# Kernel tuning notes

Hardware: AMD Instinct MI355X
Metric: run time of the kernel (lower is better)

The kernel has to match this reference:

```python
import jax, jax.numpy as jnp
import numpy as np

N = 262144
C = 81
NUM_HARD = 32768


def setup_inputs() -> dict:
    key = jax.random.key(0)
    k1, k2, k3, k4 = jax.random.split(key, 4)
    return {
        "cls_score": jax.random.normal(k1, (N, C), dtype=jnp.float32),
        "rois_label": jax.random.randint(k2, (N,), 0, C, dtype=jnp.int32),
        "bbox_pred": jax.random.normal(k3, (N, 4), dtype=jnp.float32),
        "rois_target": jax.random.normal(k4, (N, 4), dtype=jnp.float32),
        "rois_inside_ws": jnp.ones((N, 4), dtype=jnp.float32),
        "rois_outside_ws": jnp.ones((N, 4), dtype=jnp.float32),
        "num_hard": NUM_HARD,
    }


def reference(cls_score, rois_label, bbox_pred, rois_target,
              rois_inside_ws, rois_outside_ws, num_hard):
    num_classes = cls_score.shape[1]
    pos = rois_label > 0                                   # [N] bool
    num_pos = jnp.sum(pos.astype(jnp.float32))

    # --- hard-example mining on detached scores (no grad through selection) ---
    conf_p = jax.lax.stop_gradient(cls_score)              # [N, C]
    x_max = jnp.max(conf_p)                                # global scalar max (as in torch code)
    lse = jnp.log(jnp.sum(jnp.exp(conf_p - x_max), axis=1)) + x_max   # [N]
    gathered = jnp.take_along_axis(conf_p, rois_label[:, None].astype(jnp.int32), axis=1)[:, 0]
    loss_c = lse - gathered                                # [N]
    loss_c = jnp.where(pos, jnp.float32(100.0), loss_c)    # force positives in
    _, topk_idx = jax.lax.top_k(loss_c, num_hard)          # [num_hard]

    # --- weighted cross entropy on selected hard examples ---
    weight = jnp.ones((num_classes,), dtype=jnp.float32).at[0].set(num_pos / num_hard)
    sel_logits = cls_score[topk_idx]                       # [num_hard, C]
    sel_labels = rois_label[topk_idx]                      # [num_hard]
    logp = jax.nn.log_softmax(sel_logits, axis=1)
    nll = -jnp.take_along_axis(logp, sel_labels[:, None].astype(jnp.int32), axis=1)[:, 0]
    w = weight[sel_labels]
    loss_cls = jnp.sum(w * nll) / jnp.sum(w)               # torch weighted-mean CE

    # --- smooth L1 on positive rois only (masked; mean over num_pos*4 elems) ---
    diff = bbox_pred - rois_target                         # [N, 4]
    ad = jnp.abs(diff)
    sl1 = jnp.where(ad < 1.0, 0.5 * diff * diff, ad - 0.5)
    posf = pos.astype(sl1.dtype)[:, None]
    loss_box = jnp.sum(sl1 * posf) / (num_pos * 4.0)

    return loss_cls, loss_box
```

## Files before the change

kernel.cpp:

```cpp
#include <hip/hip_runtime.h>

#define NROWS 262144
#define NCLS  81
#define NTILES 4096
#define TILE_FLOATS 5184
#define KEY100 0xC2C80000u

__device__ __forceinline__ unsigned mono(float f) {
    unsigned u = __float_as_uint(f);
    return (u & 0x80000000u) ? ~u : (u | 0x80000000u);
}

__device__ __forceinline__ void gload_lds16(const void* g, void* l) {
    __builtin_amdgcn_global_load_lds(
        (const __attribute__((address_space(1))) unsigned int*)g,
        (__attribute__((address_space(3))) unsigned int*)l,
        16, 0, 0);
}

__global__ __launch_bounds__(256) void row_kernel(
        const float* __restrict__ cls, const int* __restrict__ label,
        const float* __restrict__ bpred, const float* __restrict__ btgt,
        float4* __restrict__ partial)
{
    __shared__ float sm[TILE_FLOATS];
    __shared__ unsigned ru[3][4];
    __shared__ float rf[3][4];

    const int t = threadIdx.x;
    const int lane = t & 63, wid = t >> 6;
    const int blk = blockIdx.x;
    const int row = t >> 2, j = t & 3;

    {
        const float4* src = (const float4*)(cls + (size_t)blk * TILE_FLOATS);
        #pragma unroll
        for (int jj = 0; jj < 5; ++jj) {
            int base = jj*256 + wid*64;
            gload_lds16((const void*)(src + base + lane), (void*)((float4*)sm + base));
        }
        if (t < 16)
            gload_lds16((const void*)(src + 1280 + lane), (void*)((float4*)sm + 1280));
    }

    int myLbl = label[blk*64 + row];
    float bsum = 0.f;
    {
        int gi = blk*256 + t;
        float p = bpred[gi], q = btgt[gi];
        if (myLbl > 0) {
            float d = p - q, ad = fabsf(d);
            bsum = (ad < 1.f) ? 0.5f*d*d : ad - 0.5f;
        }
    }
    __syncthreads();

    const float* rp = sm + row * NCLS;
    float s = 0.f;
    for (int i = j; i < NCLS; i += 4) s += __expf(rp[i]);
    s += __shfl_xor(s, 1);
    s += __shfl_xor(s, 2);

    unsigned pcnt = 0, gcnt = 0, ecnt = 0;
    float gtv = 0.f, pnv = 0.f;
    if (j == 0) {
        float lse = __logf(s);
        bool pos = myLbl > 0;
        float nll = lse - rp[myLbl];
        unsigned kk = mono(pos ? 100.0f : nll);
        pcnt = pos ? 1u : 0u;
        gcnt = (kk > KEY100) ? 1u : 0u;
        ecnt = (!pos && kk == KEY100) ? 1u : 0u;
        gtv  = (kk > KEY100) ? nll : 0.f;
        pnv  = pos ? nll : 0.f;
    }
    #pragma unroll
    for (int off = 32; off; off >>= 1) {
        pcnt += __shfl_xor(pcnt, off);
        gcnt += __shfl_xor(gcnt, off);
        ecnt += __shfl_xor(ecnt, off);
        gtv  += __shfl_xor(gtv, off);
        pnv  += __shfl_xor(pnv, off);
        bsum += __shfl_xor(bsum, off);
    }
    if (lane == 0) {
        ru[0][wid] = pcnt; ru[1][wid] = gcnt; ru[2][wid] = ecnt;
        rf[0][wid] = gtv;  rf[1][wid] = pnv;  rf[2][wid] = bsum;
    }
    __syncthreads();
    if (t == 0) {
        unsigned np = ru[0][0]+ru[0][1]+ru[0][2]+ru[0][3];
        unsigned ng = ru[1][0]+ru[1][1]+ru[1][2]+ru[1][3];
        unsigned ne = ru[2][0]+ru[2][1]+ru[2][2]+ru[2][3];
        float gt = rf[0][0]+rf[0][1]+rf[0][2]+rf[0][3];
        float pn = rf[1][0]+rf[1][1]+rf[1][2]+rf[1][3];
        float bx = rf[2][0]+rf[2][1]+rf[2][2]+rf[2][3];
        partial[blk] = make_float4(__uint_as_float(np | (ng<<8) | (ne<<16)), gt, pn, bx);
    }
}

__device__ void scan_desc_64k_1024(const unsigned* hist, unsigned k,
                                   unsigned* outB, unsigned* outRem,
                                   unsigned* wsum )
{
    const int t = threadIdx.x, lane = t & 63, wid = t >> 6;
    unsigned sum = 0;
    for (int j = 0; j < 64; ++j) sum += hist[65535 - (t*64 + j)];
    unsigned inc = sum;
    #pragma unroll
    for (int off = 1; off < 64; off <<= 1) {
        unsigned v = __shfl_up(inc, off);
        if (lane >= off) inc += v;
    }
    if (lane == 63) wsum[wid] = inc;
    __syncthreads();
    unsigned woff = 0;
    for (int w = 0; w < wid; ++w) woff += wsum[w];
    unsigned running = woff + inc - sum;
    for (int j = 0; j < 64; ++j) {
        unsigned bkt = 65535u - (unsigned)(t*64 + j);
        unsigned c = hist[bkt];
        if (running < k && running + c >= k) { *outB = bkt; *outRem = k - running; }
        running += c;
    }
}

__global__ __launch_bounds__(1024) void finalize_kernel(
        const float* __restrict__ cls, const int* __restrict__ label,
        const float4* __restrict__ partial, const int* __restrict__ d_num_hard,
        unsigned* __restrict__ hist, float* __restrict__ nllbuf,
        float* __restrict__ out)
{
    const int t = threadIdx.x, lane = t & 63, wid = t >> 6;
    __shared__ unsigned wNp[16], wNg[16], wNe[16];
    __shared__ float wPn[16], wGt[16], wBx[16];
    __shared__ unsigned sCross, sCumBefore;
    __shared__ float sFull, sPartial;
    __shared__ float sm[TILE_FLOATS];
    __shared__ float snll[64];
    __shared__ int slbl[64];

    unsigned npI[4]; float pnI[4];
    unsigned npS = 0, ngS = 0, neS = 0;
    float gtS = 0.f, pnS = 0.f, bxS = 0.f;
    #pragma unroll
    for (int i = 0; i < 4; ++i) {
        float4 v = partial[t*4 + i];
        unsigned c = __float_as_uint(v.x);
        npI[i] = c & 255u; pnI[i] = v.z;
        npS += npI[i]; ngS += (c >> 8) & 255u; neS += (c >> 16) & 255u;
        gtS += v.y; pnS += v.z; bxS += v.w;
    }
    unsigned incNp = npS; float incPn = pnS;
    #pragma unroll
    for (int off = 1; off < 64; off <<= 1) {
        unsigned v = __shfl_up(incNp, off);
        float    f = __shfl_up(incPn, off);
        if (lane >= off) { incNp += v; incPn += f; }
    }
    #pragma unroll
    for (int off = 32; off; off >>= 1) {
        ngS += __shfl_xor(ngS, off); neS += __shfl_xor(neS, off);
        gtS += __shfl_xor(gtS, off); bxS += __shfl_xor(bxS, off);
    }
    if (lane == 63) { wNp[wid] = incNp; wPn[wid] = incPn; }
    if (lane == 0)  { wNg[wid] = ngS; wNe[wid] = neS; wGt[wid] = gtS; wBx[wid] = bxS; }
    __syncthreads();

    unsigned NP = 0, NG = 0, NE = 0; float GT = 0.f, BX = 0.f;
    unsigned npOff = 0; float pnOff = 0.f;
    for (int w = 0; w < 16; ++w) {
        NP += wNp[w]; NG += wNg[w]; NE += wNe[w]; GT += wGt[w]; BX += wBx[w];
        if (w < wid) { npOff += wNp[w]; pnOff += wPn[w]; }
    }
    const unsigned k = (unsigned)(*d_num_hard);
    const bool fast = (NG < k) && (NG + NP >= k) && (NE == 0);

    if (fast) {
        const unsigned need = k - NG;
        unsigned cum = npOff + incNp - npS;
        float    fl  = pnOff + incPn - pnS;
        #pragma unroll
        for (int i = 0; i < 4; ++i) {
            if (cum < need && cum + npI[i] >= need) {
                sCross = (unsigned)(t*4 + i); sCumBefore = cum; sFull = fl;
            }
            cum += npI[i]; fl += pnI[i];
        }
        __syncthreads();

        {
            const float4* src = (const float4*)(cls + (size_t)sCross * TILE_FLOATS);
            float4* dst = (float4*)sm;
            dst[t] = src[t];
            if (t < 272) dst[t + 1024] = src[t + 1024];
            if (t < 64) slbl[t] = label[(int)sCross*64 + t];
        }
        __syncthreads();

        {
            const int brow = t >> 4, bj = t & 15;
            const float* rp = sm + brow * NCLS;
            float s = 0.f;
            for (int i = bj; i < NCLS; i += 16) s += __expf(rp[i]);
            s += __shfl_xor(s, 1);
            s += __shfl_xor(s, 2);
            s += __shfl_xor(s, 4);
            s += __shfl_xor(s, 8);
            if (bj == 0) snll[brow] = __logf(s) - rp[slbl[brow]];
        }
        __syncthreads();

        if (t < 64) {
            int lbl = slbl[t];
            bool pos = lbl > 0;
            unsigned long long m = __ballot(pos);
            unsigned rank = (unsigned)__popcll(m & ((1ull << t) - 1ull));
            unsigned rem = need - sCumBefore;
            float c = (pos && rank < rem) ? snll[t] : 0.f;
            #pragma unroll
            for (int off = 32; off; off >>= 1) c += __shfl_xor(c, off);
            if (t == 0) sPartial = c;
        }
        __syncthreads();
        if (t == 0) {
            float wgt0 = (float)NP / (float)k;
            out[0] = (wgt0*GT + sFull + sPartial) / (wgt0*NG + (float)need);
            out[1] = BX / ((float)NP * 4.0f);
        }
        return;
    }

    __shared__ unsigned wsum[16];
    __shared__ unsigned sB1, sKrem, sTkey, sNeed;
    __shared__ unsigned wEq[16];
    __shared__ float r1[16], r2[16];
    __syncthreads();

    for (int r = t; r < NROWS; r += 1024) {
        const float* rp = cls + (size_t)r * NCLS;
        float ssum = 0.f;
        for (int cix = 0; cix < NCLS; ++cix) ssum += __expf(rp[cix]);
        nllbuf[r] = __logf(ssum) - rp[label[r]];
    }
    __syncthreads();

    for (int i = t; i < 65536; i += 1024) hist[i] = 0u;
    __syncthreads();
    for (int base = 0; base < NROWS; base += 1024) {
        int r = base + t;
        unsigned key = mono(label[r] > 0 ? 100.0f : nllbuf[r]);
        unsigned bkt = key >> 16;
        unsigned long long active = __ballot(1);
        while (active) {
            int leader = (int)__builtin_ctzll(active);
            unsigned lb = __shfl(bkt, leader);
            unsigned long long grp = __ballot(bkt == lb) & active;
            if (lane == leader) atomicAdd(&hist[lb], (unsigned)__popcll(grp));
            active &= ~grp;
        }
    }
    __syncthreads();
    scan_desc_64k_1024(hist, k, &sB1, &sKrem, wsum);
    __syncthreads();

    for (int i = t; i < 65536; i += 1024) hist[i] = 0u;
    __syncthreads();
    for (int base = 0; base < NROWS; base += 1024) {
        int r = base + t;
        unsigned key = mono(label[r] > 0 ? 100.0f : nllbuf[r]);
        bool in = (key >> 16) == sB1;
        unsigned bkt = key & 0xFFFFu;
        unsigned long long active = __ballot(in);
        while (active) {
            int leader = (int)__builtin_ctzll(active);
            unsigned lb = __shfl(bkt, leader);
            unsigned long long grp = __ballot(in && bkt == lb) & active;
            if (lane == leader) atomicAdd(&hist[lb], (unsigned)__popcll(grp));
            active &= ~grp;
        }
    }
    __syncthreads();
    scan_desc_64k_1024(hist, sKrem, &sTkey, &sNeed, wsum);
    __syncthreads();
    if (t == 0) sTkey = (sB1 << 16) | sTkey;
    __syncthreads();

    const unsigned tkey = sTkey, need = sNeed;
    const float wgt0 = (float)NP / (float)k;
    float accN = 0.f, accW = 0.f;
    unsigned running = 0;
    for (int base = 0; base < NROWS; base += 1024) {
        int r = base + t;
        int lbl = label[r]; float v = nllbuf[r];
        unsigned key = mono(lbl > 0 ? 100.0f : v);
        bool eq = (key == tkey);
        unsigned long long b = __ballot(eq);
        if (lane == 0) wEq[wid] = (unsigned)__popcll(b);
        __syncthreads();
        unsigned woff = 0, chunkTotal = 0;
        for (int w = 0; w < 16; ++w) {
            chunkTotal += wEq[w];
            if (w < wid) woff += wEq[w];
        }
        unsigned rank = running + woff + (unsigned)__popcll(b & ((1ull << lane) - 1ull));
        bool sel = (key > tkey) || (eq && rank < need);
        if (sel) { float wg = (lbl == 0) ? wgt0 : 1.f; accN += wg * v; accW += wg; }
        running += chunkTotal;
        __syncthreads();
    }
    #pragma unroll
    for (int off = 32; off; off >>= 1) {
        accN += __shfl_xor(accN, off);
        accW += __shfl_xor(accW, off);
    }
    if (lane == 0) { r1[wid] = accN; r2[wid] = accW; }
    __syncthreads();
    if (t == 0) {
        float N = 0.f, W = 0.f;
        for (int w = 0; w < 16; ++w) { N += r1[w]; W += r2[w]; }
        out[0] = N / W;
        out[1] = BX / ((float)NP * 4.0f);
    }
}

extern "C" void kernel_launch(void* const* d_in, const int* in_sizes, int n_in,
                              void* d_out, int out_size, void* d_ws, size_t ws_size,
                              hipStream_t stream) {
    const float* cls   = (const float*)d_in[0];
    const int*   label = (const int*)d_in[1];
    const float* bpred = (const float*)d_in[2];
    const float* btgt  = (const float*)d_in[3];
    const int*   nh    = (const int*)d_in[6];
    float* out = (float*)d_out;

    char* ws = (char*)d_ws;
    float4*   partial = (float4*)(ws);
    unsigned* hist    = (unsigned*)(ws + 65536);
    float*    nllbuf  = (float*)(ws + 65536 + 262144);

    row_kernel<<<NTILES, 256, 0, stream>>>(cls, label, bpred, btgt, partial);
    finalize_kernel<<<1, 1024, 0, stream>>>(cls, label, partial, nh,
                                            hist, nllbuf, out);
}
```

Baseline: 29.14 us.

## Split row-tile LDS loads per wave and overlap compute without block barriers

```diff
diff --git a/kernel.cpp b/kernel.cpp
--- a/kernel.cpp
+++ b/kernel.cpp
@@ -24,79 +24,96 @@
         float4* __restrict__ partial)
 {
     __shared__ float sm[TILE_FLOATS];
-    __shared__ unsigned ru[3][4];
-    __shared__ float rf[3][4];
 
     const int t = threadIdx.x;
     const int lane = t & 63, wid = t >> 6;
     const int blk = blockIdx.x;
-    const int row = t >> 2, j = t & 3;
+
+    const int gi = blk*256 + t;
+    const float pbox = bpred[gi], qbox = btgt[gi];
+    const int rowh1 = wid*16 + (lane >> 3);
+    const int rowh2 = rowh1 + 8;
+    const int lblA = label[blk*64 + rowh1];
+    const int lblB = label[blk*64 + rowh2];
+    const int lblBox = label[blk*64 + (t >> 2)];
 
     {
-        const float4* src = (const float4*)(cls + (size_t)blk * TILE_FLOATS);
-        #pragma unroll
-        for (int jj = 0; jj < 5; ++jj) {
-            int base = jj*256 + wid*64;
-            gload_lds16((const void*)(src + base + lane), (void*)((float4*)sm + base));
-        }
-        if (t < 16)
-            gload_lds16((const void*)(src + 1280 + lane), (void*)((float4*)sm + 1280));
-    }
-
-    int myLbl = label[blk*64 + row];
-    float bsum = 0.f;
-    {
-        int gi = blk*256 + t;
-        float p = bpred[gi], q = btgt[gi];
-        if (myLbl > 0) {
-            float d = p - q, ad = fabsf(d);
-            bsum = (ad < 1.f) ? 0.5f*d*d : ad - 0.5f;
-        }
-    }
-    __syncthreads();
-
-    const float* rp = sm + row * NCLS;
-    float s = 0.f;
-    for (int i = j; i < NCLS; i += 4) s += __expf(rp[i]);
-    s += __shfl_xor(s, 1);
-    s += __shfl_xor(s, 2);
-
+        const float4* srcA = (const float4*)(cls + (size_t)blk * TILE_FLOATS) + wid*324;
+        float4* dstA = (float4*)sm + wid*324;
+        gload_lds16((const void*)(srcA + lane),       (void*)(dstA));
+        gload_lds16((const void*)(srcA + 64 + lane),  (void*)(dstA + 64));
+        if (lane < 34)
+            gload_lds16((const void*)(srcA + 128 + lane), (void*)(dstA + 128));
+        const float4* srcB = srcA + 162;
+        float4* dstB = dstA + 162;
+        gload_lds16((const void*)(srcB + lane),       (void*)(dstB));
+        gload_lds16((const void*)(srcB + 64 + lane),  (void*)(dstB + 64));
+        if (lane < 34)
+            gload_lds16((const void*)(srcB + 128 + lane), (void*)(dstB + 128));
+    }
+
+    const int j = lane & 7;
     unsigned pcnt = 0, gcnt = 0, ecnt = 0;
     float gtv = 0.f, pnv = 0.f;
-    if (j == 0) {
-        float lse = __logf(s);
-        bool pos = myLbl > 0;
-        float nll = lse - rp[myLbl];
-        unsigned kk = mono(pos ? 100.0f : nll);
-        pcnt = pos ? 1u : 0u;
-        gcnt = (kk > KEY100) ? 1u : 0u;
-        ecnt = (!pos && kk == KEY100) ? 1u : 0u;
-        gtv  = (kk > KEY100) ? nll : 0.f;
-        pnv  = pos ? nll : 0.f;
-    }
+
+    asm volatile("s_waitcnt vmcnt(3)" ::: "memory");
+    __builtin_amdgcn_sched_barrier(0);
+    {
+        const float* rp = sm + rowh1 * NCLS;
+        float s = 0.f;
+        #pragma unroll
+        for (int i = 0; i < 10; ++i) s += __expf(rp[j + 8*i]);
+        if (j == 0) s += __expf(rp[80]);
+        s += __shfl_xor(s, 1); s += __shfl_xor(s, 2); s += __shfl_xor(s, 4);
+        if (j == 0) {
+            float nll = __logf(s) - rp[lblA];
+            bool pos = lblA > 0;
+            unsigned kk = mono(pos ? 100.0f : nll);
+            pcnt += pos ? 1u : 0u;
+            gcnt += (kk > KEY100) ? 1u : 0u;
+            ecnt += (!pos && kk == KEY100) ? 1u : 0u;
+            gtv  += (kk > KEY100) ? nll : 0.f;
+            pnv  += pos ? nll : 0.f;
+        }
+    }
+
+    asm volatile("s_waitcnt vmcnt(0)" ::: "memory");
+    __builtin_amdgcn_sched_barrier(0);
+    {
+        const float* rp = sm + rowh2 * NCLS;
+        float s = 0.f;
+        #pragma unroll
+        for (int i = 0; i < 10; ++i) s += __expf(rp[j + 8*i]);
+        if (j == 0) s += __expf(rp[80]);
+        s += __shfl_xor(s, 1); s += __shfl_xor(s, 2); s += __shfl_xor(s, 4);
+        if (j == 0) {
+            float nll = __logf(s) - rp[lblB];
+            bool pos = lblB > 0;
+            unsigned kk = mono(pos ? 100.0f : nll);
+            pcnt += pos ? 1u : 0u;
+            gcnt += (kk > KEY100) ? 1u : 0u;
+            ecnt += (!pos && kk == KEY100) ? 1u : 0u;
+            gtv  += (kk > KEY100) ? nll : 0.f;
+            pnv  += pos ? nll : 0.f;
+        }
+    }
+
+    float bsum = 0.f;
+    if (lblBox > 0) {
+        float d = pbox - qbox, ad = fabsf(d);
+        bsum = (ad < 1.f) ? 0.5f*d*d : ad - 0.5f;
+    }
+
+    unsigned cnt = pcnt | (gcnt << 8) | (ecnt << 16);
     #pragma unroll
     for (int off = 32; off; off >>= 1) {
-        pcnt += __shfl_xor(pcnt, off);
-        gcnt += __shfl_xor(gcnt, off);
-        ecnt += __shfl_xor(ecnt, off);
+        cnt  += __shfl_xor(cnt, off);
         gtv  += __shfl_xor(gtv, off);
         pnv  += __shfl_xor(pnv, off);
         bsum += __shfl_xor(bsum, off);
     }
-    if (lane == 0) {
-        ru[0][wid] = pcnt; ru[1][wid] = gcnt; ru[2][wid] = ecnt;
-        rf[0][wid] = gtv;  rf[1][wid] = pnv;  rf[2][wid] = bsum;
-    }
-    __syncthreads();
-    if (t == 0) {
-        unsigned np = ru[0][0]+ru[0][1]+ru[0][2]+ru[0][3];
-        unsigned ng = ru[1][0]+ru[1][1]+ru[1][2]+ru[1][3];
-        unsigned ne = ru[2][0]+ru[2][1]+ru[2][2]+ru[2][3];
-        float gt = rf[0][0]+rf[0][1]+rf[0][2]+rf[0][3];
-        float pn = rf[1][0]+rf[1][1]+rf[1][2]+rf[1][3];
-        float bx = rf[2][0]+rf[2][1]+rf[2][2]+rf[2][3];
-        partial[blk] = make_float4(__uint_as_float(np | (ng<<8) | (ne<<16)), gt, pn, bx);
-    }
+    if (lane == 0)
+        partial[blk*4 + wid] = make_float4(__uint_as_float(cnt), gtv, pnv, bsum);
 }
 
 __device__ void scan_desc_64k_1024(const unsigned* hist, unsigned k,
@@ -145,11 +162,17 @@
     float gtS = 0.f, pnS = 0.f, bxS = 0.f;
     #pragma unroll
     for (int i = 0; i < 4; ++i) {
-        float4 v = partial[t*4 + i];
-        unsigned c = __float_as_uint(v.x);
-        npI[i] = c & 255u; pnI[i] = v.z;
-        npS += npI[i]; ngS += (c >> 8) & 255u; neS += (c >> 16) & 255u;
-        gtS += v.y; pnS += v.z; bxS += v.w;
+        unsigned npw = 0, ngw = 0, new_ = 0; float gtw = 0.f, pnw = 0.f, bxw = 0.f;
+        #pragma unroll
+        for (int w2 = 0; w2 < 4; ++w2) {
+            float4 v = partial[(size_t)(t*4 + i)*4 + w2];
+            unsigned c = __float_as_uint(v.x);
+            npw += c & 255u; ngw += (c >> 8) & 255u; new_ += (c >> 16) & 255u;
+            gtw += v.y; pnw += v.z; bxw += v.w;
+        }
+        npI[i] = npw; pnI[i] = pnw;
+        npS += npw; ngS += ngw; neS += new_;
+        gtS += gtw; pnS += pnw; bxS += bxw;
     }
     unsigned incNp = npS; float incPn = pnS;
     #pragma unroll
@@ -336,8 +359,8 @@
 
     char* ws = (char*)d_ws;
     float4*   partial = (float4*)(ws);
-    unsigned* hist    = (unsigned*)(ws + 65536);
-    float*    nllbuf  = (float*)(ws + 65536 + 262144);
+    unsigned* hist    = (unsigned*)(ws + 262144);
+    float*    nllbuf  = (float*)(ws + 524288);
 
     row_kernel<<<NTILES, 256, 0, stream>>>(cls, label, bpred, btgt, partial);
     finalize_kernel<<<1, 1024, 0, stream>>>(cls, label, partial, nh,
```

Result: slower. 33.17 us (+13.8%).
